# Performance work log

Hardware: AMD Instinct MI355X
Metric: run time of the kernel (lower is better)

The kernel has to match this reference:

```python
import jax, jax.numpy as jnp
import numpy as np

B, C, U, LEN, K = 32, 16, 16, 128, 4  # batch, channels, units, image side, cheb order
POWERS = K + 1


def _path_chebyshev(n, k):
    """Chebyshev polynomials T_0..T_k of the rescaled normalized Laplacian of an
    undirected path graph with n nodes. Returns [k+1, n, n] float32."""
    A = np.zeros((n, n), dtype=np.float64)
    A[np.arange(n - 1), np.arange(1, n)] = 1.0
    A = A + A.T
    d = A.sum(axis=1)
    dinv = 1.0 / np.sqrt(d)
    L = np.eye(n) - dinv[:, None] * A * dinv[None, :]   # normalized Laplacian
    Lt = L - np.eye(n)                                   # rescaled: 2L/lambda_max - I, lambda_max=2
    T = [np.eye(n), Lt]
    for _ in range(2, k + 1):
        T.append(2.0 * Lt @ T[-1] - T[-2])
    return np.stack(T[: k + 1]).astype(np.float32)


def setup_inputs() -> dict:
    key = jax.random.key(0)
    kx, kc = jax.random.split(key)
    x = jax.random.normal(kx, (B, C, LEN, LEN), dtype=jnp.float32)
    coefs = 0.001 * jax.random.normal(kc, (POWERS, POWERS, C, U), dtype=jnp.float32)
    cheb = jnp.asarray(_path_chebyshev(LEN, K))  # same graph for both axes
    return {"x": x, "coefs": coefs, "cheb1": cheb, "cheb2": cheb}


def reference(x, coefs, cheb1, cheb2):
    # out[b,u,p,q] = sum_{k1,k2,c,h,w} coefs[k1,k2,c,u] * cheb1[k1,h,p] * x[b,c,h,w] * cheb2[k2,w,q]
    t1 = jnp.einsum('bchw,khp->bkcpw', x, cheb1)        # apply cheb1 along H
    s = jnp.einsum('bkcpw,klcu->blupw', t1, coefs)      # contract k1 and channels
    out = jnp.einsum('blupw,lwq->bupq', s, cheb2)       # apply cheb2 along W, contract k2
    return out
```

## Files before the change

kernel.cpp:

```cpp
#include <hip/hip_runtime.h>
#include <hip/hip_bf16.h>

#define LEN 128
#define NB 32
#define NC 16
#define NU 16
#define NK 5
#define KC 80
#define KCP 96
#define LUN 80

typedef unsigned int uint32;
typedef unsigned short ushort16;
typedef __attribute__((ext_vector_type(8))) short bf16x8;
typedef __attribute__((ext_vector_type(4))) float f32x4;

#define MFMA(a, b, c) __builtin_amdgcn_mfma_f32_16x16x32_bf16(a, b, c, 0, 0, 0)

static __device__ inline ushort16 f2bf(float f) {
    union { float f; uint32 u; } v; v.f = f;
    uint32 u = v.u;
    uint32 r = (u + 0x7fffu + ((u >> 16) & 1u)) >> 16;
    return (ushort16)r;
}
static __device__ inline uint32 pkbf(float a, float b) {
    return (uint32)f2bf(a) | ((uint32)f2bf(b) << 16);
}
static __device__ inline bf16x8 frag16(const void* p) {
    return *(const bf16x8*)p;
}

__global__ __launch_bounds__(256) void k0_prep(const float* __restrict__ coefs,
                                               const float* __restrict__ cheb1,
                                               const float* __restrict__ cheb2,
                                               ushort16* __restrict__ cheb1T,
                                               ushort16* __restrict__ cheb2T,
                                               ushort16* __restrict__ coefTT) {
    int i = blockIdx.x * 256 + threadIdx.x;
    if (i < 81920) {
        int kp = i >> 7, h = i & 127;
        int k = kp >> 7, p = kp & 127;
        cheb1T[i] = f2bf(cheb1[(k * LEN + h) * LEN + p]);
    } else if (i < 163840) {
        int j = i - 81920;
        int q = j / 640, t = j % 640;
        int l = t >> 7, w = t & 127;
        cheb2T[j] = f2bf(cheb2[(l * LEN + w) * LEN + q]);
    } else if (i < 171520) {
        int j = i - 163840;
        int lu = j / KCP, kc = j % KCP;
        int l = lu >> 4, u = lu & 15, k = kc >> 4, c = kc & 15;
        coefTT[j] = (kc < KC) ? f2bf(coefs[((k * NK + l) * NC + c) * NU + u]) : (ushort16)0;
    }
}

__global__ __launch_bounds__(256, 2) void k1_mfma(const float* __restrict__ x,
                                                  const uint32* __restrict__ cheb1T,
                                                  ushort16* __restrict__ t1, int b0) {
    __shared__ __align__(16) uint32 Xs[128 * 68];
    __shared__ __align__(16) uint32 As[160 * 68];
    const int c = blockIdx.x, bl = blockIdx.y, b = b0 + bl;
    const int tid = threadIdx.x;
    const int lane = tid & 63, wave = tid >> 6;
    const int m16 = lane & 15, g = lane >> 4;
    const int wm = wave >> 1, wn = wave & 1;

    {
        const float* xp = x + (size_t)(b * NC + c) * (LEN * LEN);
        int w = tid & 127, hg = tid >> 7;
        #pragma unroll 4
        for (int i = 0; i < 32; ++i) {
            int h2 = hg * 32 + i;
            float f0 = xp[(2 * h2) * LEN + w];
            float f1 = xp[(2 * h2 + 1) * LEN + w];
            Xs[w * 68 + h2] = pkbf(f0, f1);
        }
    }

    for (int pass = 0; pass < 4; ++pass) {
        __syncthreads();
        #pragma unroll
        for (int i = 0; i < 10; ++i) {
            int it = tid + i * 256;
            int r = it >> 4, cc = it & 15;
            uint4 v = *(const uint4*)(cheb1T + (size_t)(pass * 160 + r) * 64 + cc * 4);
            *(uint4*)(As + r * 68 + cc * 4) = v;
        }
        __syncthreads();

        f32x4 acc[4][5];
        #pragma unroll
        for (int mi = 0; mi < 4; ++mi)
            #pragma unroll
            for (int ni = 0; ni < 5; ++ni) acc[mi][ni] = (f32x4)0.f;

        #pragma unroll
        for (int ks = 0; ks < 4; ++ks) {
            bf16x8 Af[4], Bf[5];
            #pragma unroll
            for (int mi = 0; mi < 4; ++mi)
                Af[mi] = frag16(Xs + (wm * 64 + mi * 16 + m16) * 68 + ks * 16 + g * 4);
            #pragma unroll
            for (int ni = 0; ni < 5; ++ni)
                Bf[ni] = frag16(As + (wn * 80 + ni * 16 + m16) * 68 + ks * 16 + g * 4);
            #pragma unroll
            for (int mi = 0; mi < 4; ++mi)
                #pragma unroll
                for (int ni = 0; ni < 5; ++ni)
                    acc[mi][ni] = MFMA(Af[mi], Bf[ni], acc[mi][ni]);
        }

        #pragma unroll
        for (int ni = 0; ni < 5; ++ni) {
            int kp = pass * 160 + wn * 80 + ni * 16 + m16;
            int k = kp >> 7, p = kp & 127;
            size_t base = (((size_t)(bl * LEN + p) * NK + k) * NC + c) * LEN;
            #pragma unroll
            for (int mi = 0; mi < 4; ++mi) {
                int w0 = wm * 64 + mi * 16 + g * 4;
                uint2 d;
                d.x = pkbf(acc[mi][ni][0], acc[mi][ni][1]);
                d.y = pkbf(acc[mi][ni][2], acc[mi][ni][3]);
                *(uint2*)((ushort16*)t1 + base + w0) = d;
            }
        }
    }
}

__global__ __launch_bounds__(256, 2) void k2_mfma(const ushort16* __restrict__ t1,
                                                  const ushort16* __restrict__ coefTT,
                                                  const ushort16* __restrict__ cheb2T,
                                                  float* __restrict__ out, int b0) {
    __shared__ __align__(16) uint32 sm[2 * 128 * 52];
    const int pg = blockIdx.x, bl = blockIdx.y, b = b0 + bl;
    const int tid = threadIdx.x;
    const int lane = tid & 63, wave = tid >> 6;
    const int n16 = lane & 15, g = lane >> 4;

    {
        const uint32* t1u = (const uint32*)(t1 + (size_t)(bl * LEN + 2 * pg) * (KC * LEN));
        #pragma unroll
        for (int i = 0; i < 5; ++i) {
            int it = tid + i * 256;
            int p_i = (it >= 640) ? 1 : 0;
            int rem = it - 640 * p_i;
            int kc2 = rem >> 4, wq = rem & 15;
            const uint32* src = t1u + p_i * 5120 + kc2 * 128 + wq * 4;
            uint4 Av = *(const uint4*)(src);
            uint4 Bv = *(const uint4*)(src + 64);
            uint32* dst = sm + (p_i * 128 + wq * 8) * 52 + kc2;
            const uint32* av = (const uint32*)&Av;
            const uint32* bv = (const uint32*)&Bv;
            #pragma unroll
            for (int j = 0; j < 4; ++j) {
                dst[(2 * j) * 52]     = (av[j] & 0xffffu) | (bv[j] << 16);
                dst[(2 * j + 1) * 52] = (av[j] >> 16) | (bv[j] & 0xffff0000u);
            }
        }
        for (int j = tid; j < 2048; j += 256) {
            int row = j >> 3, d = j & 7;
            sm[row * 52 + 40 + d] = 0;
        }
    }
    __syncthreads();

    const int wp = wave >> 1, ww = wave & 1;
    f32x4 acc[4][5];
    #pragma unroll
    for (int mi = 0; mi < 4; ++mi)
        #pragma unroll
        for (int ni = 0; ni < 5; ++ni) acc[mi][ni] = (f32x4)0.f;

    #pragma unroll
    for (int ks = 0; ks < 3; ++ks) {
        bf16x8 Af[4], Bf[5];
        #pragma unroll
        for (int mi = 0; mi < 4; ++mi)
            Af[mi] = frag16(sm + (wp * 128 + ww * 64 + mi * 16 + n16) * 52 + ks * 16 + g * 4);
        #pragma unroll
        for (int ni = 0; ni < 5; ++ni)
            Bf[ni] = frag16(coefTT + (size_t)(ni * 16 + n16) * KCP + ks * 32 + g * 8);
        #pragma unroll
        for (int mi = 0; mi < 4; ++mi)
            #pragma unroll
            for (int ni = 0; ni < 5; ++ni)
                acc[mi][ni] = MFMA(Af[mi], Bf[ni], acc[mi][ni]);
    }
    __syncthreads();

    {
        ushort16* A3 = (ushort16*)sm;
        #pragma unroll
        for (int mi = 0; mi < 4; ++mi)
            #pragma unroll
            for (int ni = 0; ni < 5; ++ni) {
                int lu = ni * 16 + n16, u = lu & 15, l = lu >> 4;
                int w0 = ww * 64 + mi * 16 + g * 4;
                int pu = wp * 16 + u;
                uint2 d;
                d.x = pkbf(acc[mi][ni][0], acc[mi][ni][1]);
                d.y = pkbf(acc[mi][ni][2], acc[mi][ni][3]);
                *(uint2*)(A3 + pu * 648 + l * 128 + w0) = d;
            }
    }
    __syncthreads();

    const ushort16* A3r = (const ushort16*)sm;
    f32x4 c3[2][2];
    c3[0][0] = (f32x4)0.f; c3[0][1] = (f32x4)0.f;
    c3[1][0] = (f32x4)0.f; c3[1][1] = (f32x4)0.f;
    #pragma unroll 5
    for (int ks = 0; ks < 20; ++ks) {
        bf16x8 Af2[2], Bf2[2];
        #pragma unroll
        for (int mi = 0; mi < 2; ++mi)
            Af2[mi] = frag16(A3r + (mi * 16 + n16) * 648 + ks * 32 + g * 8);
        #pragma unroll
        for (int nt = 0; nt < 2; ++nt)
            Bf2[nt] = frag16(cheb2T + (size_t)(wave * 32 + nt * 16 + n16) * 640 + ks * 32 + g * 8);
        #pragma unroll
        for (int mi = 0; mi < 2; ++mi)
            #pragma unroll
            for (int nt = 0; nt < 2; ++nt)
                c3[mi][nt] = MFMA(Af2[mi], Bf2[nt], c3[mi][nt]);
    }

    #pragma unroll
    for (int mi = 0; mi < 2; ++mi)
        #pragma unroll
        for (int nt = 0; nt < 2; ++nt)
            #pragma unroll
            for (int r = 0; r < 4; ++r) {
                int u = g * 4 + r;
                int q = wave * 32 + nt * 16 + n16;
                out[(((size_t)(b * NU + u)) * LEN + (2 * pg + mi)) * LEN + q] = c3[mi][nt][r];
            }
}

extern "C" void kernel_launch(void* const* d_in, const int* in_sizes, int n_in,
                              void* d_out, int out_size, void* d_ws, size_t ws_size,
                              hipStream_t stream) {
    const float* x     = (const float*)d_in[0];
    const float* coefs = (const float*)d_in[1];
    const float* cheb1 = (const float*)d_in[2];
    const float* cheb2 = (const float*)d_in[3];
    float* out = (float*)d_out;

    const size_t aux_bytes = 163840 + 163840 + 15360;
    size_t aux_off = (ws_size - aux_bytes) & ~(size_t)255;
    ushort16* cheb1T = (ushort16*)((char*)d_ws + aux_off);
    ushort16* cheb2T = cheb1T + 81920;
    ushort16* coefTT = cheb2T + 81920;
    ushort16* t1 = (ushort16*)d_ws;

    const size_t per_b = (size_t)NK * NC * LEN * LEN * sizeof(ushort16);
    int chunk = (int)(aux_off / per_b);
    if (chunk < 1) chunk = 1;
    if (chunk > NB) chunk = NB;

    hipLaunchKernelGGL(k0_prep, dim3((171520 + 255) / 256), dim3(256), 0, stream,
                       coefs, cheb1, cheb2, cheb1T, cheb2T, coefTT);
    for (int b0 = 0; b0 < NB; b0 += chunk) {
        int cb = (NB - b0 < chunk) ? (NB - b0) : chunk;
        hipLaunchKernelGGL(k1_mfma, dim3(NC, cb), dim3(256), 0, stream,
                           x, (const uint32*)cheb1T, t1, b0);
        hipLaunchKernelGGL(k2_mfma, dim3(64, cb), dim3(256), 0, stream,
                           t1, coefTT, cheb2T, out, b0);
    }
}
```

Measured before the change: 174.2 us.

## Store intermediate in k-interleaved layout so stage two reads fragments directly

Changes the intermediate t1 layout to [b,p,w,kpair,c] with the Chebyshev order interleaved and padded to 6. The second kernel can then load MFMA A fragments straight from global memory, removing its shared-memory transpose and repack step. The first kernel now reads cheb1 fragments directly from global memory instead of staging them in LDS, and uses a smaller LDS footprint so occupancy can rise to three blocks. The grid order is swapped so that batch is the fastest-varying dimension. In exchange, the first kernel's stores become scattered 4-byte writes, and the padding enlarges the intermediate from 80 to 96 k-channels.

New measurement: 292.5 us. +67.9%, slower.

```diff
diff --git a/kernel.cpp b/kernel.cpp
--- a/kernel.cpp
+++ b/kernel.cpp
@@ -1,45 +1,51 @@
 #include <hip/hip_runtime.h>
-#include <hip/hip_bf16.h>
 
 #define LEN 128
 #define NB 32
 #define NC 16
 #define NU 16
 #define NK 5
-#define KC 80
-#define KCP 96
+#define KQ 96
+#define KQD 48
 #define LUN 80
 
 typedef unsigned int uint32;
-typedef unsigned short ushort16;
+typedef unsigned short u16;
 typedef __attribute__((ext_vector_type(8))) short bf16x8;
 typedef __attribute__((ext_vector_type(4))) float f32x4;
 
 #define MFMA(a, b, c) __builtin_amdgcn_mfma_f32_16x16x32_bf16(a, b, c, 0, 0, 0)
 
-static __device__ inline ushort16 f2bf(float f) {
+static __device__ inline u16 f2bf(float f) {
     union { float f; uint32 u; } v; v.f = f;
     uint32 u = v.u;
-    uint32 r = (u + 0x7fffu + ((u >> 16) & 1u)) >> 16;
-    return (ushort16)r;
+    return (u16)((u + 0x7fffu + ((u >> 16) & 1u)) >> 16);
 }
 static __device__ inline uint32 pkbf(float a, float b) {
     return (uint32)f2bf(a) | ((uint32)f2bf(b) << 16);
 }
-static __device__ inline bf16x8 frag16(const void* p) {
-    return *(const bf16x8*)p;
+static __device__ inline bf16x8 frag16(const void* p) { return *(const bf16x8*)p; }
+static __device__ inline bf16x8 frag4(const uint32* p) {
+    union { uint32 u[4]; bf16x8 v; } t;
+    t.u[0] = p[0]; t.u[1] = p[1]; t.u[2] = p[2]; t.u[3] = p[3];
+    return t.v;
+}
+static __device__ inline bf16x8 frag4s(const uint32* p, int stride) {
+    union { uint32 u[4]; bf16x8 v; } t;
+    t.u[0] = p[0]; t.u[1] = p[stride]; t.u[2] = p[2 * stride]; t.u[3] = p[3 * stride];
+    return t.v;
 }
 
 __global__ __launch_bounds__(256) void k0_prep(const float* __restrict__ coefs,
                                                const float* __restrict__ cheb1,
                                                const float* __restrict__ cheb2,
-                                               ushort16* __restrict__ cheb1T,
-                                               ushort16* __restrict__ cheb2T,
-                                               ushort16* __restrict__ coefTT) {
+                                               u16* __restrict__ cheb1T,
+                                               u16* __restrict__ cheb2T,
+                                               u16* __restrict__ coefTT) {
     int i = blockIdx.x * 256 + threadIdx.x;
     if (i < 81920) {
-        int kp = i >> 7, h = i & 127;
-        int k = kp >> 7, p = kp & 127;
+        int r = i >> 7, h = i & 127;
+        int k = r >> 7, p = r & 127;
         cheb1T[i] = f2bf(cheb1[(k * LEN + h) * LEN + p]);
     } else if (i < 163840) {
         int j = i - 81920;
@@ -48,176 +54,135 @@
         cheb2T[j] = f2bf(cheb2[(l * LEN + w) * LEN + q]);
     } else if (i < 171520) {
         int j = i - 163840;
-        int lu = j / KCP, kc = j % KCP;
-        int l = lu >> 4, u = lu & 15, k = kc >> 4, c = kc & 15;
-        coefTT[j] = (kc < KC) ? f2bf(coefs[((k * NK + l) * NC + c) * NU + u]) : (ushort16)0;
-    }
-}
-
-__global__ __launch_bounds__(256, 2) void k1_mfma(const float* __restrict__ x,
+        int lu = j / KQ, kap = j % KQ;
+        int l = lu >> 4, u = lu & 15;
+        int k2 = kap >> 5, rem = kap & 31, c = rem >> 1, tt = rem & 1;
+        int k = 2 * k2 + tt;
+        coefTT[j] = (k < NK) ? f2bf(coefs[((k * NK + l) * NC + c) * NU + u]) : (u16)0;
+    }
+}
+
+__global__ __launch_bounds__(256, 3) void k1_mfma(const float* __restrict__ x,
                                                   const uint32* __restrict__ cheb1T,
-                                                  ushort16* __restrict__ t1, int b0) {
-    __shared__ __align__(16) uint32 Xs[128 * 68];
-    __shared__ __align__(16) uint32 As[160 * 68];
-    const int c = blockIdx.x, bl = blockIdx.y, b = b0 + bl;
+                                                  uint32* __restrict__ t1d, int b0) {
+    __shared__ uint32 Xs2[64 * 132];
+    const int bl = blockIdx.x, c = blockIdx.y, b = b0 + bl;
+    const int tid = threadIdx.x;
+    const int lane = tid & 63;
+    const int m16 = lane & 15, g = lane >> 4;
+    const int wave = tid >> 6, wm = wave >> 1, wn = wave & 1;
+
+    {
+        const float* xp = x + (size_t)(b * NC + c) * (LEN * LEN);
+        int w = tid & 127, hb = (tid >> 7) * 32;
+        #pragma unroll 8
+        for (int i = 0; i < 32; ++i) {
+            int h2 = hb + i;
+            Xs2[h2 * 132 + w] = pkbf(xp[(2 * h2) * LEN + w], xp[(2 * h2 + 1) * LEN + w]);
+        }
+    }
+    __syncthreads();
+
+    for (int pass = 0; pass < 4; ++pass) {
+        const int P0 = pass * 32 + wm * 16;
+        f32x4 acc[5][4];
+        #pragma unroll
+        for (int k = 0; k < 5; ++k)
+            #pragma unroll
+            for (int ni = 0; ni < 4; ++ni) acc[k][ni] = (f32x4)0.f;
+
+        #pragma unroll
+        for (int ks = 0; ks < 4; ++ks) {
+            bf16x8 Af[5], Bf[4];
+            #pragma unroll
+            for (int k = 0; k < 5; ++k)
+                Af[k] = frag16(cheb1T + (size_t)(k * 128 + P0 + m16) * 64 + ks * 16 + g * 4);
+            #pragma unroll
+            for (int ni = 0; ni < 4; ++ni)
+                Bf[ni] = frag4s(Xs2 + (ks * 16 + g * 4) * 132 + wn * 64 + ni * 16 + m16, 132);
+            #pragma unroll
+            for (int k = 0; k < 5; ++k)
+                #pragma unroll
+                for (int ni = 0; ni < 4; ++ni)
+                    acc[k][ni] = MFMA(Af[k], Bf[ni], acc[k][ni]);
+        }
+
+        #pragma unroll
+        for (int ni = 0; ni < 4; ++ni) {
+            int w = wn * 64 + ni * 16 + m16;
+            #pragma unroll
+            for (int r = 0; r < 4; ++r) {
+                int p = P0 + g * 4 + r;
+                uint32* dst = t1d + ((size_t)(bl * LEN + p) * LEN + w) * KQD + c;
+                dst[0]  = pkbf(acc[0][ni][r], acc[1][ni][r]);
+                dst[16] = pkbf(acc[2][ni][r], acc[3][ni][r]);
+                dst[32] = pkbf(acc[4][ni][r], 0.f);
+            }
+        }
+    }
+}
+
+__global__ __launch_bounds__(256, 3) void k2_mfma(const uint32* __restrict__ t1d,
+                                                  const u16* __restrict__ coefTT,
+                                                  const u16* __restrict__ cheb2T,
+                                                  float* __restrict__ out, int b0) {
+    __shared__ uint32 A3[32 * 326];
+    const int bl = blockIdx.x, pg = blockIdx.y, b = b0 + bl;
     const int tid = threadIdx.x;
     const int lane = tid & 63, wave = tid >> 6;
     const int m16 = lane & 15, g = lane >> 4;
-    const int wm = wave >> 1, wn = wave & 1;
-
-    {
-        const float* xp = x + (size_t)(b * NC + c) * (LEN * LEN);
-        int w = tid & 127, hg = tid >> 7;
-        #pragma unroll 4
-        for (int i = 0; i < 32; ++i) {
-            int h2 = hg * 32 + i;
-            float f0 = xp[(2 * h2) * LEN + w];
-            float f1 = xp[(2 * h2 + 1) * LEN + w];
-            Xs[w * 68 + h2] = pkbf(f0, f1);
-        }
-    }
-
-    for (int pass = 0; pass < 4; ++pass) {
-        __syncthreads();
-        #pragma unroll
-        for (int i = 0; i < 10; ++i) {
-            int it = tid + i * 256;
-            int r = it >> 4, cc = it & 15;
-            uint4 v = *(const uint4*)(cheb1T + (size_t)(pass * 160 + r) * 64 + cc * 4);
-            *(uint4*)(As + r * 68 + cc * 4) = v;
-        }
-        __syncthreads();
-
-        f32x4 acc[4][5];
-        #pragma unroll
-        for (int mi = 0; mi < 4; ++mi)
-            #pragma unroll
-            for (int ni = 0; ni < 5; ++ni) acc[mi][ni] = (f32x4)0.f;
-
-        #pragma unroll
-        for (int ks = 0; ks < 4; ++ks) {
-            bf16x8 Af[4], Bf[5];
-            #pragma unroll
-            for (int mi = 0; mi < 4; ++mi)
-                Af[mi] = frag16(Xs + (wm * 64 + mi * 16 + m16) * 68 + ks * 16 + g * 4);
-            #pragma unroll
-            for (int ni = 0; ni < 5; ++ni)
-                Bf[ni] = frag16(As + (wn * 80 + ni * 16 + m16) * 68 + ks * 16 + g * 4);
-            #pragma unroll
-            for (int mi = 0; mi < 4; ++mi)
-                #pragma unroll
-                for (int ni = 0; ni < 5; ++ni)
-                    acc[mi][ni] = MFMA(Af[mi], Bf[ni], acc[mi][ni]);
-        }
-
-        #pragma unroll
-        for (int ni = 0; ni < 5; ++ni) {
-            int kp = pass * 160 + wn * 80 + ni * 16 + m16;
-            int k = kp >> 7, p = kp & 127;
-            size_t base = (((size_t)(bl * LEN + p) * NK + k) * NC + c) * LEN;
-            #pragma unroll
-            for (int mi = 0; mi < 4; ++mi) {
-                int w0 = wm * 64 + mi * 16 + g * 4;
-                uint2 d;
-                d.x = pkbf(acc[mi][ni][0], acc[mi][ni][1]);
-                d.y = pkbf(acc[mi][ni][2], acc[mi][ni][3]);
-                *(uint2*)((ushort16*)t1 + base + w0) = d;
-            }
-        }
-    }
-}
-
-__global__ __launch_bounds__(256, 2) void k2_mfma(const ushort16* __restrict__ t1,
-                                                  const ushort16* __restrict__ coefTT,
-                                                  const ushort16* __restrict__ cheb2T,
-                                                  float* __restrict__ out, int b0) {
-    __shared__ __align__(16) uint32 sm[2 * 128 * 52];
-    const int pg = blockIdx.x, bl = blockIdx.y, b = b0 + bl;
-    const int tid = threadIdx.x;
-    const int lane = tid & 63, wave = tid >> 6;
-    const int n16 = lane & 15, g = lane >> 4;
-
-    {
-        const uint32* t1u = (const uint32*)(t1 + (size_t)(bl * LEN + 2 * pg) * (KC * LEN));
-        #pragma unroll
-        for (int i = 0; i < 5; ++i) {
-            int it = tid + i * 256;
-            int p_i = (it >= 640) ? 1 : 0;
-            int rem = it - 640 * p_i;
-            int kc2 = rem >> 4, wq = rem & 15;
-            const uint32* src = t1u + p_i * 5120 + kc2 * 128 + wq * 4;
-            uint4 Av = *(const uint4*)(src);
-            uint4 Bv = *(const uint4*)(src + 64);
-            uint32* dst = sm + (p_i * 128 + wq * 8) * 52 + kc2;
-            const uint32* av = (const uint32*)&Av;
-            const uint32* bv = (const uint32*)&Bv;
-            #pragma unroll
-            for (int j = 0; j < 4; ++j) {
-                dst[(2 * j) * 52]     = (av[j] & 0xffffu) | (bv[j] << 16);
-                dst[(2 * j + 1) * 52] = (av[j] >> 16) | (bv[j] & 0xffff0000u);
-            }
-        }
-        for (int j = tid; j < 2048; j += 256) {
-            int row = j >> 3, d = j & 7;
-            sm[row * 52 + 40 + d] = 0;
-        }
-    }
-    __syncthreads();
-
     const int wp = wave >> 1, ww = wave & 1;
+    const int p = 2 * pg + wp;
+
+    const uint32* arow = t1d + (size_t)(bl * LEN + p) * LEN * KQD;
     f32x4 acc[4][5];
     #pragma unroll
     for (int mi = 0; mi < 4; ++mi)
         #pragma unroll
-        for (int ni = 0; ni < 5; ++ni) acc[mi][ni] = (f32x4)0.f;
+        for (int n = 0; n < 5; ++n) acc[mi][n] = (f32x4)0.f;
 
     #pragma unroll
     for (int ks = 0; ks < 3; ++ks) {
         bf16x8 Af[4], Bf[5];
         #pragma unroll
+        for (int mi = 0; mi < 4; ++mi) {
+            int w = ww * 64 + mi * 16 + m16;
+            Af[mi] = frag16(arow + (size_t)w * KQD + ks * 16 + g * 4);
+        }
+        #pragma unroll
+        for (int n = 0; n < 5; ++n)
+            Bf[n] = frag16(coefTT + (size_t)(n * 16 + m16) * KQ + ks * 32 + g * 8);
+        #pragma unroll
         for (int mi = 0; mi < 4; ++mi)
-            Af[mi] = frag16(sm + (wp * 128 + ww * 64 + mi * 16 + n16) * 52 + ks * 16 + g * 4);
-        #pragma unroll
-        for (int ni = 0; ni < 5; ++ni)
-            Bf[ni] = frag16(coefTT + (size_t)(ni * 16 + n16) * KCP + ks * 32 + g * 8);
-        #pragma unroll
-        for (int mi = 0; mi < 4; ++mi)
-            #pragma unroll
-            for (int ni = 0; ni < 5; ++ni)
-                acc[mi][ni] = MFMA(Af[mi], Bf[ni], acc[mi][ni]);
-    }
+            #pragma unroll
+            for (int n = 0; n < 5; ++n)
+                acc[mi][n] = MFMA(Af[mi], Bf[n], acc[mi][n]);
+    }
+
+    #pragma unroll
+    for (int mi = 0; mi < 4; ++mi)
+        #pragma unroll
+        for (int n = 0; n < 5; ++n) {
+            int lu = n * 16 + m16, l = lu >> 4, u = lu & 15;
+            int w0 = ww * 64 + mi * 16 + g * 4;
+            uint32* d = A3 + (wp * 16 + u) * 326 + l * 64 + (w0 >> 1);
+            d[0] = pkbf(acc[mi][n][0], acc[mi][n][1]);
+            d[1] = pkbf(acc[mi][n][2], acc[mi][n][3]);
+        }
     __syncthreads();
 
-    {
-        ushort16* A3 = (ushort16*)sm;
-        #pragma unroll
-        for (int mi = 0; mi < 4; ++mi)
-            #pragma unroll
-            for (int ni = 0; ni < 5; ++ni) {
-                int lu = ni * 16 + n16, u = lu & 15, l = lu >> 4;
-                int w0 = ww * 64 + mi * 16 + g * 4;
-                int pu = wp * 16 + u;
-                uint2 d;
-                d.x = pkbf(acc[mi][ni][0], acc[mi][ni][1]);
-                d.y = pkbf(acc[mi][ni][2], acc[mi][ni][3]);
-                *(uint2*)(A3 + pu * 648 + l * 128 + w0) = d;
-            }
-    }
-    __syncthreads();
-
-    const ushort16* A3r = (const ushort16*)sm;
     f32x4 c3[2][2];
     c3[0][0] = (f32x4)0.f; c3[0][1] = (f32x4)0.f;
     c3[1][0] = (f32x4)0.f; c3[1][1] = (f32x4)0.f;
-    #pragma unroll 5
+    #pragma unroll 4
     for (int ks = 0; ks < 20; ++ks) {
         bf16x8 Af2[2], Bf2[2];
         #pragma unroll
         for (int mi = 0; mi < 2; ++mi)
-            Af2[mi] = frag16(A3r + (mi * 16 + n16) * 648 + ks * 32 + g * 8);
+            Af2[mi] = frag4(A3 + (mi * 16 + m16) * 326 + ks * 16 + g * 4);
         #pragma unroll
         for (int nt = 0; nt < 2; ++nt)
-            Bf2[nt] = frag16(cheb2T + (size_t)(wave * 32 + nt * 16 + n16) * 640 + ks * 32 + g * 8);
+            Bf2[nt] = frag16(cheb2T + (size_t)(wave * 32 + nt * 16 + m16) * 640 + ks * 32 + g * 8);
         #pragma unroll
         for (int mi = 0; mi < 2; ++mi)
             #pragma unroll
@@ -232,7 +197,7 @@
             #pragma unroll
             for (int r = 0; r < 4; ++r) {
                 int u = g * 4 + r;
-                int q = wave * 32 + nt * 16 + n16;
+                int q = wave * 32 + nt * 16 + m16;
                 out[(((size_t)(b * NU + u)) * LEN + (2 * pg + mi)) * LEN + q] = c3[mi][nt][r];
             }
 }
@@ -248,12 +213,12 @@
 
     const size_t aux_bytes = 163840 + 163840 + 15360;
     size_t aux_off = (ws_size - aux_bytes) & ~(size_t)255;
-    ushort16* cheb1T = (ushort16*)((char*)d_ws + aux_off);
-    ushort16* cheb2T = cheb1T + 81920;
-    ushort16* coefTT = cheb2T + 81920;
-    ushort16* t1 = (ushort16*)d_ws;
-
-    const size_t per_b = (size_t)NK * NC * LEN * LEN * sizeof(ushort16);
+    u16* cheb1T = (u16*)((char*)d_ws + aux_off);
+    u16* cheb2T = cheb1T + 81920;
+    u16* coefTT = cheb2T + 81920;
+    uint32* t1d = (uint32*)d_ws;
+
+    const size_t per_b = (size_t)LEN * LEN * KQD * 4;
     int chunk = (int)(aux_off / per_b);
     if (chunk < 1) chunk = 1;
     if (chunk > NB) chunk = NB;
@@ -262,9 +227,9 @@
                        coefs, cheb1, cheb2, cheb1T, cheb2T, coefTT);
     for (int b0 = 0; b0 < NB; b0 += chunk) {
         int cb = (NB - b0 < chunk) ? (NB - b0) : chunk;
-        hipLaunchKernelGGL(k1_mfma, dim3(NC, cb), dim3(256), 0, stream,
-                           x, (const uint32*)cheb1T, t1, b0);
-        hipLaunchKernelGGL(k2_mfma, dim3(64, cb), dim3(256), 0, stream,
-                           t1, coefTT, cheb2T, out, b0);
-    }
-}
+        hipLaunchKernelGGL(k1_mfma, dim3(cb, NC), dim3(256), 0, stream,
+                           x, (const uint32*)cheb1T, t1d, b0);
+        hipLaunchKernelGGL(k2_mfma, dim3(cb, 64), dim3(256), 0, stream,
+                           t1d, coefTT, cheb2T, out, b0);
+    }
+}
```

## Pre-transpose x to bf16, split k1 across output-row tiles, pad k2 LDS

Applied to the files above, without the earlier changes.

A new kernel transposes and packs x into a bf16 [w][h] layout with coalesced float4 reads through a shared tile. k1 then drops its LDS staging and multi-pass loop: each block handles one 160-row slab of cheb1 and reads A/B fragments straight from global memory. This gives 4x more blocks and allows occupancy 3. k2 changes its LDS row strides from 52/648 to 53/326 words with scalar dword fragment loads, to avoid bank conflicts. The cost is an extra kernel launch, an extra round trip of x through memory, and redundant global reads of fragments in k1.

New measurement: 204.9 us. +17.7%, slower.

```diff
diff --git a/kernel.cpp b/kernel.cpp
--- a/kernel.cpp
+++ b/kernel.cpp
@@ -1,5 +1,4 @@
 #include <hip/hip_runtime.h>
-#include <hip/hip_bf16.h>
 
 #define LEN 128
 #define NB 32
@@ -11,35 +10,37 @@
 #define LUN 80
 
 typedef unsigned int uint32;
-typedef unsigned short ushort16;
+typedef unsigned short u16;
 typedef __attribute__((ext_vector_type(8))) short bf16x8;
 typedef __attribute__((ext_vector_type(4))) float f32x4;
 
 #define MFMA(a, b, c) __builtin_amdgcn_mfma_f32_16x16x32_bf16(a, b, c, 0, 0, 0)
 
-static __device__ inline ushort16 f2bf(float f) {
+static __device__ inline u16 f2bf(float f) {
     union { float f; uint32 u; } v; v.f = f;
     uint32 u = v.u;
-    uint32 r = (u + 0x7fffu + ((u >> 16) & 1u)) >> 16;
-    return (ushort16)r;
+    return (u16)((u + 0x7fffu + ((u >> 16) & 1u)) >> 16);
 }
 static __device__ inline uint32 pkbf(float a, float b) {
     return (uint32)f2bf(a) | ((uint32)f2bf(b) << 16);
 }
-static __device__ inline bf16x8 frag16(const void* p) {
-    return *(const bf16x8*)p;
+static __device__ inline bf16x8 frag16(const void* p) { return *(const bf16x8*)p; }
+static __device__ inline bf16x8 frag4(const uint32* p) {
+    union { uint32 u[4]; bf16x8 v; } t;
+    t.u[0] = p[0]; t.u[1] = p[1]; t.u[2] = p[2]; t.u[3] = p[3];
+    return t.v;
 }
 
 __global__ __launch_bounds__(256) void k0_prep(const float* __restrict__ coefs,
                                                const float* __restrict__ cheb1,
                                                const float* __restrict__ cheb2,
-                                               ushort16* __restrict__ cheb1T,
-                                               ushort16* __restrict__ cheb2T,
-                                               ushort16* __restrict__ coefTT) {
+                                               u16* __restrict__ cheb1T,
+                                               u16* __restrict__ cheb2T,
+                                               u16* __restrict__ coefTT) {
     int i = blockIdx.x * 256 + threadIdx.x;
     if (i < 81920) {
-        int kp = i >> 7, h = i & 127;
-        int k = kp >> 7, p = kp & 127;
+        int r = i >> 7, h = i & 127;
+        int k = r >> 7, p = r & 127;
         cheb1T[i] = f2bf(cheb1[(k * LEN + h) * LEN + p]);
     } else if (i < 163840) {
         int j = i - 81920;
@@ -50,92 +51,105 @@
         int j = i - 163840;
         int lu = j / KCP, kc = j % KCP;
         int l = lu >> 4, u = lu & 15, k = kc >> 4, c = kc & 15;
-        coefTT[j] = (kc < KC) ? f2bf(coefs[((k * NK + l) * NC + c) * NU + u]) : (ushort16)0;
-    }
-}
-
-__global__ __launch_bounds__(256, 2) void k1_mfma(const float* __restrict__ x,
+        coefTT[j] = (kc < KCP && kc < KC) ? f2bf(coefs[((k * NK + l) * NC + c) * NU + u]) : (u16)0;
+    }
+}
+
+__global__ __launch_bounds__(256) void k0_xT(const float* __restrict__ x,
+                                             uint32* __restrict__ xT) {
+    __shared__ float Ls[32][131];
+    const int bc = blockIdx.x;
+    const float* xp = x + (size_t)bc * (LEN * LEN);
+    uint32* op = xT + (size_t)bc * (LEN * 64);
+    const int tid = threadIdx.x;
+
+    for (int slab = 0; slab < 4; ++slab) {
+        __syncthreads();
+        {
+            int h = tid >> 3, wq = tid & 7;
+            const float* src = xp + (size_t)(slab * 32 + h) * LEN + wq * 16;
+            #pragma unroll
+            for (int j = 0; j < 4; ++j) {
+                float4 v = *(const float4*)(src + 4 * j);
+                Ls[h][wq * 16 + 4 * j + 0] = v.x;
+                Ls[h][wq * 16 + 4 * j + 1] = v.y;
+                Ls[h][wq * 16 + 4 * j + 2] = v.z;
+                Ls[h][wq * 16 + 4 * j + 3] = v.w;
+            }
+        }
+        __syncthreads();
+        {
+            int h2 = tid & 15, wg = tid >> 4;
+            #pragma unroll
+            for (int ww = 0; ww < 8; ++ww) {
+                int w = wg * 8 + ww;
+                op[(size_t)w * 64 + slab * 16 + h2] = pkbf(Ls[2 * h2][w], Ls[2 * h2 + 1][w]);
+            }
+        }
+    }
+}
+
+__global__ __launch_bounds__(256, 3) void k1_mfma(const uint32* __restrict__ xT,
                                                   const uint32* __restrict__ cheb1T,
-                                                  ushort16* __restrict__ t1, int b0) {
-    __shared__ __align__(16) uint32 Xs[128 * 68];
-    __shared__ __align__(16) uint32 As[160 * 68];
-    const int c = blockIdx.x, bl = blockIdx.y, b = b0 + bl;
+                                                  u16* __restrict__ t1, int b0) {
+    const int kpw = blockIdx.y, zz = blockIdx.z;
+    const int c = blockIdx.x + 8 * (zz & 1);
+    const int bl = zz >> 1;
     const int tid = threadIdx.x;
     const int lane = tid & 63, wave = tid >> 6;
     const int m16 = lane & 15, g = lane >> 4;
     const int wm = wave >> 1, wn = wave & 1;
 
-    {
-        const float* xp = x + (size_t)(b * NC + c) * (LEN * LEN);
-        int w = tid & 127, hg = tid >> 7;
-        #pragma unroll 4
-        for (int i = 0; i < 32; ++i) {
-            int h2 = hg * 32 + i;
-            float f0 = xp[(2 * h2) * LEN + w];
-            float f1 = xp[(2 * h2 + 1) * LEN + w];
-            Xs[w * 68 + h2] = pkbf(f0, f1);
-        }
-    }
-
-    for (int pass = 0; pass < 4; ++pass) {
-        __syncthreads();
-        #pragma unroll
-        for (int i = 0; i < 10; ++i) {
-            int it = tid + i * 256;
-            int r = it >> 4, cc = it & 15;
-            uint4 v = *(const uint4*)(cheb1T + (size_t)(pass * 160 + r) * 64 + cc * 4);
-            *(uint4*)(As + r * 68 + cc * 4) = v;
-        }
-        __syncthreads();
-
-        f32x4 acc[4][5];
-        #pragma unroll
-        for (int mi = 0; mi < 4; ++mi)
-            #pragma unroll
-            for (int ni = 0; ni < 5; ++ni) acc[mi][ni] = (f32x4)0.f;
-
-        #pragma unroll
-        for (int ks = 0; ks < 4; ++ks) {
-            bf16x8 Af[4], Bf[5];
-            #pragma unroll
-            for (int mi = 0; mi < 4; ++mi)
-                Af[mi] = frag16(Xs + (wm * 64 + mi * 16 + m16) * 68 + ks * 16 + g * 4);
+    const uint32* xrow = xT + (size_t)((b0 + bl) * NC + c) * (LEN * 64);
+
+    f32x4 acc[4][5];
+    #pragma unroll
+    for (int mi = 0; mi < 4; ++mi)
+        #pragma unroll
+        for (int ni = 0; ni < 5; ++ni) acc[mi][ni] = (f32x4)0.f;
+
+    #pragma unroll
+    for (int ks = 0; ks < 4; ++ks) {
+        bf16x8 Af[4], Bf[5];
+        #pragma unroll
+        for (int mi = 0; mi < 4; ++mi)
+            Af[mi] = frag16(xrow + (size_t)(wm * 64 + mi * 16 + m16) * 64 + ks * 16 + g * 4);
+        #pragma unroll
+        for (int ni = 0; ni < 5; ++ni)
+            Bf[ni] = frag16(cheb1T + (size_t)(kpw * 160 + wn * 80 + ni * 16 + m16) * 64 + ks * 16 + g * 4);
+        #pragma unroll
+        for (int mi = 0; mi < 4; ++mi)
             #pragma unroll
             for (int ni = 0; ni < 5; ++ni)
-                Bf[ni] = frag16(As + (wn * 80 + ni * 16 + m16) * 68 + ks * 16 + g * 4);
-            #pragma unroll
-            for (int mi = 0; mi < 4; ++mi)
-                #pragma unroll
-                for (int ni = 0; ni < 5; ++ni)
-                    acc[mi][ni] = MFMA(Af[mi], Bf[ni], acc[mi][ni]);
-        }
-
-        #pragma unroll
-        for (int ni = 0; ni < 5; ++ni) {
-            int kp = pass * 160 + wn * 80 + ni * 16 + m16;
-            int k = kp >> 7, p = kp & 127;
-            size_t base = (((size_t)(bl * LEN + p) * NK + k) * NC + c) * LEN;
-            #pragma unroll
-            for (int mi = 0; mi < 4; ++mi) {
-                int w0 = wm * 64 + mi * 16 + g * 4;
-                uint2 d;
-                d.x = pkbf(acc[mi][ni][0], acc[mi][ni][1]);
-                d.y = pkbf(acc[mi][ni][2], acc[mi][ni][3]);
-                *(uint2*)((ushort16*)t1 + base + w0) = d;
-            }
-        }
-    }
-}
-
-__global__ __launch_bounds__(256, 2) void k2_mfma(const ushort16* __restrict__ t1,
-                                                  const ushort16* __restrict__ coefTT,
-                                                  const ushort16* __restrict__ cheb2T,
+                acc[mi][ni] = MFMA(Af[mi], Bf[ni], acc[mi][ni]);
+    }
+
+    #pragma unroll
+    for (int ni = 0; ni < 5; ++ni) {
+        int kp = kpw * 160 + wn * 80 + ni * 16 + m16;
+        int k = kp >> 7, p = kp & 127;
+        size_t base = (((size_t)(bl * LEN + p) * NK + k) * NC + c) * LEN;
+        #pragma unroll
+        for (int mi = 0; mi < 4; ++mi) {
+            int w0 = wm * 64 + mi * 16 + g * 4;
+            uint2 d;
+            d.x = pkbf(acc[mi][ni][0], acc[mi][ni][1]);
+            d.y = pkbf(acc[mi][ni][2], acc[mi][ni][3]);
+            *(uint2*)(t1 + base + w0) = d;
+        }
+    }
+}
+
+__global__ __launch_bounds__(256, 2) void k2_mfma(const u16* __restrict__ t1,
+                                                  const u16* __restrict__ coefTT,
+                                                  const u16* __restrict__ cheb2T,
                                                   float* __restrict__ out, int b0) {
-    __shared__ __align__(16) uint32 sm[2 * 128 * 52];
+    __shared__ uint32 sm[256 * 53];
     const int pg = blockIdx.x, bl = blockIdx.y, b = b0 + bl;
     const int tid = threadIdx.x;
     const int lane = tid & 63, wave = tid >> 6;
     const int n16 = lane & 15, g = lane >> 4;
+    const int wp = wave >> 1, ww = wave & 1;
 
     {
         const uint32* t1u = (const uint32*)(t1 + (size_t)(bl * LEN + 2 * pg) * (KC * LEN));
@@ -148,73 +162,70 @@
             const uint32* src = t1u + p_i * 5120 + kc2 * 128 + wq * 4;
             uint4 Av = *(const uint4*)(src);
             uint4 Bv = *(const uint4*)(src + 64);
-            uint32* dst = sm + (p_i * 128 + wq * 8) * 52 + kc2;
+            uint32* dst = sm + (p_i * 128 + wq * 8) * 53 + kc2;
             const uint32* av = (const uint32*)&Av;
             const uint32* bv = (const uint32*)&Bv;
             #pragma unroll
             for (int j = 0; j < 4; ++j) {
-                dst[(2 * j) * 52]     = (av[j] & 0xffffu) | (bv[j] << 16);
-                dst[(2 * j + 1) * 52] = (av[j] >> 16) | (bv[j] & 0xffff0000u);
+                dst[(2 * j) * 53]     = (av[j] & 0xffffu) | (bv[j] << 16);
+                dst[(2 * j + 1) * 53] = (av[j] >> 16) | (bv[j] & 0xffff0000u);
             }
         }
         for (int j = tid; j < 2048; j += 256) {
-            int row = j >> 3, d = j & 7;
-            sm[row * 52 + 40 + d] = 0;
+            int row = j >> 3, d = 40 + (j & 7);
+            sm[row * 53 + d] = 0;
         }
     }
     __syncthreads();
 
-    const int wp = wave >> 1, ww = wave & 1;
     f32x4 acc[4][5];
     #pragma unroll
     for (int mi = 0; mi < 4; ++mi)
         #pragma unroll
-        for (int ni = 0; ni < 5; ++ni) acc[mi][ni] = (f32x4)0.f;
+        for (int n = 0; n < 5; ++n) acc[mi][n] = (f32x4)0.f;
 
     #pragma unroll
     for (int ks = 0; ks < 3; ++ks) {
         bf16x8 Af[4], Bf[5];
         #pragma unroll
         for (int mi = 0; mi < 4; ++mi)
-            Af[mi] = frag16(sm + (wp * 128 + ww * 64 + mi * 16 + n16) * 52 + ks * 16 + g * 4);
-        #pragma unroll
-        for (int ni = 0; ni < 5; ++ni)
-            Bf[ni] = frag16(coefTT + (size_t)(ni * 16 + n16) * KCP + ks * 32 + g * 8);
-        #pragma unroll
-        for (int mi = 0; mi < 4; ++mi)
-            #pragma unroll
-            for (int ni = 0; ni < 5; ++ni)
-                acc[mi][ni] = MFMA(Af[mi], Bf[ni], acc[mi][ni]);
+            Af[mi] = frag4(sm + (wp * 128 + ww * 64 + mi * 16 + n16) * 53 + ks * 16 + g * 4);
+        #pragma unroll
+        for (int n = 0; n < 5; ++n)
+            Bf[n] = frag16(coefTT + (size_t)(n * 16 + n16) * KCP + ks * 32 + g * 8);
+        #pragma unroll
+        for (int mi = 0; mi < 4; ++mi)
+            #pragma unroll
+            for (int n = 0; n < 5; ++n)
+                acc[mi][n] = MFMA(Af[mi], Bf[n], acc[mi][n]);
     }
     __syncthreads();
 
     {
-        ushort16* A3 = (ushort16*)sm;
-        #pragma unroll
-        for (int mi = 0; mi < 4; ++mi)
-            #pragma unroll
-            for (int ni = 0; ni < 5; ++ni) {
-                int lu = ni * 16 + n16, u = lu & 15, l = lu >> 4;
+        uint32* A3 = sm;
+        #pragma unroll
+        for (int mi = 0; mi < 4; ++mi)
+            #pragma unroll
+            for (int n = 0; n < 5; ++n) {
+                int lu = n * 16 + n16, l = lu >> 4, u = lu & 15;
                 int w0 = ww * 64 + mi * 16 + g * 4;
-                int pu = wp * 16 + u;
-                uint2 d;
-                d.x = pkbf(acc[mi][ni][0], acc[mi][ni][1]);
-                d.y = pkbf(acc[mi][ni][2], acc[mi][ni][3]);
-                *(uint2*)(A3 + pu * 648 + l * 128 + w0) = d;
+                uint32* d = A3 + (wp * 16 + u) * 326 + l * 64 + (w0 >> 1);
+                d[0] = pkbf(acc[mi][n][0], acc[mi][n][1]);
+                d[1] = pkbf(acc[mi][n][2], acc[mi][n][3]);
             }
     }
     __syncthreads();
 
-    const ushort16* A3r = (const ushort16*)sm;
+    const uint32* A3 = sm;
     f32x4 c3[2][2];
     c3[0][0] = (f32x4)0.f; c3[0][1] = (f32x4)0.f;
     c3[1][0] = (f32x4)0.f; c3[1][1] = (f32x4)0.f;
-    #pragma unroll 5
+    #pragma unroll 4
     for (int ks = 0; ks < 20; ++ks) {
         bf16x8 Af2[2], Bf2[2];
         #pragma unroll
         for (int mi = 0; mi < 2; ++mi)
-            Af2[mi] = frag16(A3r + (mi * 16 + n16) * 648 + ks * 32 + g * 8);
+            Af2[mi] = frag4(A3 + (mi * 16 + n16) * 326 + ks * 16 + g * 4);
         #pragma unroll
         for (int nt = 0; nt < 2; ++nt)
             Bf2[nt] = frag16(cheb2T + (size_t)(wave * 32 + nt * 16 + n16) * 640 + ks * 32 + g * 8);
@@ -246,24 +257,29 @@
     const float* cheb2 = (const float*)d_in[3];
     float* out = (float*)d_out;
 
-    const size_t aux_bytes = 163840 + 163840 + 15360;
-    size_t aux_off = (ws_size - aux_bytes) & ~(size_t)255;
-    ushort16* cheb1T = (ushort16*)((char*)d_ws + aux_off);
-    ushort16* cheb2T = cheb1T + 81920;
-    ushort16* coefTT = cheb2T + 81920;
-    ushort16* t1 = (ushort16*)d_ws;
-
-    const size_t per_b = (size_t)NK * NC * LEN * LEN * sizeof(ushort16);
+    const size_t xT_bytes = (size_t)NB * NC * LEN * 64 * 4;
+    const size_t aux_bytes = xT_bytes + 163840 + 163840 + 15360;
+    size_t aux_off = (ws_size > aux_bytes + 256) ? ((ws_size - aux_bytes) & ~(size_t)255) : 0;
+
+    uint32* xT  = (uint32*)((char*)d_ws + aux_off);
+    u16* cheb1T = (u16*)((char*)xT + xT_bytes);
+    u16* cheb2T = cheb1T + 81920;
+    u16* coefTT = cheb2T + 81920;
+    u16* t1 = (u16*)d_ws;
+
+    const size_t per_b = (size_t)NK * NC * LEN * LEN * sizeof(u16);
     int chunk = (int)(aux_off / per_b);
     if (chunk < 1) chunk = 1;
     if (chunk > NB) chunk = NB;
 
     hipLaunchKernelGGL(k0_prep, dim3((171520 + 255) / 256), dim3(256), 0, stream,
                        coefs, cheb1, cheb2, cheb1T, cheb2T, coefTT);
+    hipLaunchKernelGGL(k0_xT, dim3(NB * NC), dim3(256), 0, stream, x, xT);
+
     for (int b0 = 0; b0 < NB; b0 += chunk) {
         int cb = (NB - b0 < chunk) ? (NB - b0) : chunk;
-        hipLaunchKernelGGL(k1_mfma, dim3(NC, cb), dim3(256), 0, stream,
-                           x, (const uint32*)cheb1T, t1, b0);
+        hipLaunchKernelGGL(k1_mfma, dim3(8, 4, 2 * cb), dim3(256), 0, stream,
+                           xT, (const uint32*)cheb1T, t1, b0);
         hipLaunchKernelGGL(k2_mfma, dim3(64, cb), dim3(256), 0, stream,
                            t1, coefTT, cheb2T, out, b0);
     }
```
